# Performance work log

Measured on AMD Instinct MI355X. Metric: run time of the kernel, lower is better.

## Reference

```python
import jax, jax.numpy as jnp
import numpy as np

N_G = 50000   # glomeruli nodes
N_C = 100000  # immune cell nodes
D_IN = 128    # raw input feature dim
D = 64        # hidden_dim
E_GG = 800000
E_CG = 1600000
E_CC = 1600000
LN_EPS = 1e-5


def _ln(x, s, b):
    m = x.mean(-1, keepdims=True)
    v = ((x - m) ** 2).mean(-1, keepdims=True)
    return (x - m) * jax.lax.rsqrt(v + LN_EPS) * s + b


def _gcn(x, ei, ew, W, b, n):
    # PyG GCNConv: normalize=True, add_self_loops=True (self-loop weight 1)
    xt = x @ W                                   # [n, D]
    row, col = ei[0], ei[1]
    deg = jax.ops.segment_sum(ew, col, num_segments=n) + 1.0  # + self loop
    dinv = jnp.where(deg > 0, jax.lax.rsqrt(deg), 0.0)
    norm = dinv[row] * ew * dinv[col]            # [E]
    out = jax.ops.segment_sum(norm[:, None] * xt[row], col, num_segments=n)
    out = out + (dinv * dinv)[:, None] * xt      # self-loop contribution
    return out + b


def _gin(x_src, x_dst, ei, eps, W, b, n_dst):
    # PyG GINConv (bipartite): nn((1+eps)*x_dst + sum_j x_src[j]), nn = Linear+ReLU
    agg = jax.ops.segment_sum(x_src[ei[0]], ei[1], num_segments=n_dst)
    h = (1.0 + eps) * x_dst + agg
    return jax.nn.relu(h @ W + b)


def setup_inputs() -> dict:
    key = jax.random.key(0)
    ks = jax.random.split(key, 48)
    ctr = [0]
    def nk():
        k = ks[ctr[0]]; ctr[0] += 1; return k
    def w(fan_in, shape):
        return jax.random.normal(nk(), shape, jnp.float32) * (1.0 / np.sqrt(fan_in))
    inp = {}
    inp["x_glom"] = jax.random.normal(nk(), (N_G, D_IN), jnp.float32)
    inp["x_cell"] = jax.random.normal(nk(), (N_C, D_IN), jnp.float32)
    inp["edge_index_gg"] = jax.random.randint(nk(), (2, E_GG), 0, N_G)
    inp["edge_weight_gg"] = jax.random.uniform(nk(), (E_GG,), jnp.float32)
    inp["edge_index_cg"] = jnp.stack([jax.random.randint(nk(), (E_CG,), 0, N_C),
                                      jax.random.randint(nk(), (E_CG,), 0, N_G)])
    inp["edge_index_cc"] = jax.random.randint(nk(), (2, E_CC), 0, N_C)
    # initial per-node-type FC (LazyLinear -> LayerNorm -> ReLU)
    inp["W_in_g"] = w(D_IN, (D_IN, D)); inp["b_in_g"] = jnp.zeros((D,))
    inp["lnig_s"] = jnp.ones((D,));     inp["lnig_b"] = jnp.zeros((D,))
    inp["W_in_c"] = w(D_IN, (D_IN, D)); inp["b_in_c"] = jnp.zeros((D,))
    inp["lnic_s"] = jnp.ones((D,));     inp["lnic_b"] = jnp.zeros((D,))
    for l in ("1", "2"):
        inp["W_gcn" + l] = w(D, (D, D)); inp["b_gcn" + l] = jnp.zeros((D,))
        inp["eps_cg" + l] = jnp.zeros((1,))
        inp["W_cg" + l] = w(D, (D, D)); inp["b_cg" + l] = jnp.zeros((D,))
        inp["eps_cc" + l] = jnp.zeros((1,))
        inp["W_cc" + l] = w(D, (D, D)); inp["b_cc" + l] = jnp.zeros((D,))
        inp["ln" + l + "_s"] = jnp.ones((D,)); inp["ln" + l + "_b"] = jnp.zeros((D,))
    inp["W_out"] = w(D, (D, 3)); inp["b_out"] = jnp.zeros((3,))
    return inp


def reference(x_glom, x_cell, edge_index_gg, edge_weight_gg, edge_index_cg, edge_index_cc,
              W_in_g, b_in_g, lnig_s, lnig_b, W_in_c, b_in_c, lnic_s, lnic_b,
              W_gcn1, b_gcn1, eps_cg1, W_cg1, b_cg1, eps_cc1, W_cc1, b_cc1, ln1_s, ln1_b,
              W_gcn2, b_gcn2, eps_cg2, W_cg2, b_cg2, eps_cc2, W_cc2, b_cc2, ln2_s, ln2_b,
              W_out, b_out):
    # initial per-type FC (dropout identity in eval)
    xg = jax.nn.relu(_ln(x_glom @ W_in_g + b_in_g, lnig_s, lnig_b))
    xc = jax.nn.relu(_ln(x_cell @ W_in_c + b_in_c, lnic_s, lnic_b))
    # hetero MP layer 1: HeteroConv aggr='sum' over relations into each dst type
    g = _gcn(xg, edge_index_gg, edge_weight_gg, W_gcn1, b_gcn1, N_G) \
        + _gin(xc, xg, edge_index_cg, eps_cg1, W_cg1, b_cg1, N_G)
    c = _gin(xc, xc, edge_index_cc, eps_cc1, W_cc1, b_cc1, N_C)
    xg = jax.nn.relu(_ln(g, ln1_s, ln1_b))   # shared LayerNorm across node types
    xc = jax.nn.relu(_ln(c, ln1_s, ln1_b))
    # hetero MP layer 2
    g = _gcn(xg, edge_index_gg, edge_weight_gg, W_gcn2, b_gcn2, N_G) \
        + _gin(xc, xg, edge_index_cg, eps_cg2, W_cg2, b_cg2, N_G)
    c = _gin(xc, xc, edge_index_cc, eps_cc2, W_cc2, b_cc2, N_C)
    xg = jax.nn.relu(_ln(g, ln2_s, ln2_b))
    xc = jax.nn.relu(_ln(c, ln2_s, ln2_b))
    logits = xg @ W_out + b_out
    return jax.nn.softmax(logits, axis=-1)
```

## Files before the change

### kernel.cpp

```cpp
#include <hip/hip_runtime.h>
#include <hip/hip_fp16.h>

#define NG 50000
#define NC 100000
#define DIN 128
#define D 64
#define EGG 800000
#define ECG 1600000
#define ECC 1600000
#define LN_EPS 1e-5f

#define SCAN_N (2 * NG + NC)
#define E_ALL (EGG + ECG + ECC)
#define NBKT 196
#define NBLK 512
#define EPB ((E_ALL + NBLK - 1) / NBLK)

typedef _Float16 f16x8 __attribute__((ext_vector_type(8)));
typedef float f32x4 __attribute__((ext_vector_type(4)));

__device__ __forceinline__ float wave_sum64(float v) {
#pragma unroll
  for (int off = 32; off > 0; off >>= 1) v += __shfl_xor(v, off);
  return v;
}

__device__ __forceinline__ float bcast_lane(float v, int k) {
  return __int_as_float(__builtin_amdgcn_readlane(__float_as_int(v), k));
}

__device__ __forceinline__ float csr_gather_s2(
    const int* __restrict__ src, const float* __restrict__ nrm,
    const __half* __restrict__ tab, int e0, int e1, int lane) {
  int h = lane >> 5;
  int m = lane & 31;
  float ax0 = 0.f, ax1 = 0.f, ax2 = 0.f, ax3 = 0.f;
  float ay0 = 0.f, ay1 = 0.f, ay2 = 0.f, ay3 = 0.f;
  for (int e = e0; e < e1; e += 16) {
#pragma unroll
    for (int p = 0; p < 8; ++p) {
      int i0 = e + 2 * p;
      int se = src[i0];
      int so = src[i0 + 1];
      int s = h ? so : se;
      bool valid = (i0 + h) < e1;
      float w;
      if (nrm) {
        float we = nrm[i0], wo = nrm[i0 + 1];
        w = h ? wo : we;
      } else {
        w = 1.0f;
      }
      w = valid ? w : 0.0f;
      s = valid ? s : 0;
      __half2 v = *(const __half2*)(tab + (size_t)s * D + 2 * m);
      float vl = __low2float(v), vh = __high2float(v);
      switch (p & 3) {
        case 0: ax0 = fmaf(w, vl, ax0); ay0 = fmaf(w, vh, ay0); break;
        case 1: ax1 = fmaf(w, vl, ax1); ay1 = fmaf(w, vh, ay1); break;
        case 2: ax2 = fmaf(w, vl, ax2); ay2 = fmaf(w, vh, ay2); break;
        default: ax3 = fmaf(w, vl, ax3); ay3 = fmaf(w, vh, ay3); break;
      }
    }
  }
  float ax = (ax0 + ax1) + (ax2 + ax3);
  float ay = (ay0 + ay1) + (ay2 + ay3);
  ax += __shfl_xor(ax, 32);
  ay += __shfl_xor(ay, 32);
  float ev = __shfl(ax, lane >> 1);
  float od = __shfl(ay, lane >> 1);
  return (lane & 1) ? od : ev;
}

__global__ __launch_bounds__(256) void fc_in_mfma_kernel(
    const float* __restrict__ x, const float* __restrict__ W,
    const float* __restrict__ b, const float* __restrict__ s,
    const float* __restrict__ beta, __half* __restrict__ y, int n) {
  int wid = (int)(((size_t)blockIdx.x * blockDim.x + threadIdx.x) >> 6);
  int lane = threadIdx.x & 63;
  int r0 = wid * 16;
  if (r0 >= n) return;
  int lo = lane & 15;
  int hi = lane >> 4;

  f16x8 bf[4][4];
#pragma unroll
  for (int kk = 0; kk < 4; ++kk) {
    int kbase = kk * 32 + hi * 8;
#pragma unroll
    for (int t = 0; t < 4; ++t) {
      int c = t * 16 + lo;
      f16x8 v;
#pragma unroll
      for (int j = 0; j < 8; ++j)
        v[j] = (_Float16)W[(kbase + j) * 64 + c];
      bf[kk][t] = v;
    }
  }

  f32x4 acc[4];
#pragma unroll
  for (int t = 0; t < 4; ++t) acc[t] = (f32x4){0.f, 0.f, 0.f, 0.f};

  const float* xr = x + (size_t)(r0 + lo) * DIN;
#pragma unroll
  for (int kk = 0; kk < 4; ++kk) {
    int kbase = kk * 32 + hi * 8;
    float4 xa = *(const float4*)(xr + kbase);
    float4 xb = *(const float4*)(xr + kbase + 4);
    f16x8 af;
    af[0] = (_Float16)xa.x; af[1] = (_Float16)xa.y;
    af[2] = (_Float16)xa.z; af[3] = (_Float16)xa.w;
    af[4] = (_Float16)xb.x; af[5] = (_Float16)xb.y;
    af[6] = (_Float16)xb.z; af[7] = (_Float16)xb.w;
#pragma unroll
    for (int t = 0; t < 4; ++t)
      acc[t] = __builtin_amdgcn_mfma_f32_16x16x32_f16(af, bf[kk][t], acc[t], 0, 0, 0);
  }

  float bc[4], lsv[4], lbv[4];
#pragma unroll
  for (int t = 0; t < 4; ++t) {
    int c = t * 16 + lo;
    bc[t] = b[c]; lsv[t] = s[c]; lbv[t] = beta[c];
  }
#pragma unroll
  for (int reg = 0; reg < 4; ++reg) {
    float v[4];
    float s1 = 0.0f;
#pragma unroll
    for (int t = 0; t < 4; ++t) { v[t] = acc[t][reg] + bc[t]; s1 += v[t]; }
#pragma unroll
    for (int off = 1; off < 16; off <<= 1) s1 += __shfl_xor(s1, off);
    float m = s1 * (1.0f / 64.0f);
    float s2 = 0.0f;
#pragma unroll
    for (int t = 0; t < 4; ++t) { float d = v[t] - m; s2 += d * d; }
#pragma unroll
    for (int off = 1; off < 16; off <<= 1) s2 += __shfl_xor(s2, off);
    float rinv = rsqrtf(s2 * (1.0f / 64.0f) + LN_EPS);
    int r = r0 + hi * 4 + reg;
#pragma unroll
    for (int t = 0; t < 4; ++t) {
      float o = (v[t] - m) * rinv * lsv[t] + lbv[t];
      y[(size_t)r * D + t * 16 + lo] = __float2half(fmaxf(o, 0.0f));
    }
  }
}

__global__ __launch_bounds__(256) void r1_hist_kernel(
    const int* __restrict__ ei_gg, const int* __restrict__ ei_cg,
    const int* __restrict__ ei_cc, int* __restrict__ bhist,
    int* __restrict__ btot) {
  __shared__ int hist[256];
  int t = threadIdx.x;
  int k = blockIdx.x;
  hist[t] = 0;
  __syncthreads();
  int base = k * EPB;
  for (int i = t; i < EPB; i += 256) {
    int e = base + i;
    if (e >= E_ALL) break;
    int key;
    if (e < EGG) key = ei_gg[EGG + e];
    else if (e < EGG + ECG) key = NG + ei_cg[ECG + (e - EGG)];
    else key = 2 * NG + ei_cc[ECC + (e - EGG - ECG)];
    atomicAdd(&hist[key >> 10], 1);
  }
  __syncthreads();
  if (t < NBKT) {
    bhist[t * NBLK + k] = hist[t];
    atomicAdd(&btot[t], hist[t]);
  }
}

__global__ __launch_bounds__(256) void r2b_kernel(
    const int* __restrict__ btot, int* __restrict__ bbase,
    int* __restrict__ S) {
  __shared__ int sh[256];
  int t = threadIdx.x;
  int v = (t < NBKT) ? btot[t] : 0;
  sh[t] = v;
  __syncthreads();
#pragma unroll
  for (int off = 1; off < 256; off <<= 1) {
    int u = (t >= off) ? sh[t - off] : 0;
    __syncthreads();
    sh[t] += u;
    __syncthreads();
  }
  if (t < NBKT) bbase[t] = sh[t] - v;
  if (t == 255) { bbase[NBKT] = sh[255]; S[SCAN_N] = sh[255]; }
}

__global__ __launch_bounds__(512) void r2c_kernel(
    const int* __restrict__ bhist, const int* __restrict__ bbase,
    int* __restrict__ base) {
  int b = blockIdx.x;
  int t = threadIdx.x;
  int lane = t & 63, wv = t >> 6;
  int v = bhist[b * NBLK + t];
  int sc = v;
#pragma unroll
  for (int off = 1; off < 64; off <<= 1) {
    int u = __shfl_up(sc, off);
    if (lane >= off) sc += u;
  }
  __shared__ int ws[8];
  if (lane == 63) ws[wv] = sc;
  __syncthreads();
  int wb = 0;
  for (int i = 0; i < wv; ++i) wb += ws[i];
  base[b * NBLK + t] = bbase[b] + wb + sc - v;
}

__global__ __launch_bounds__(256) void r3_scatter_kernel(
    const int* __restrict__ ei_gg, const float* __restrict__ ew_gg,
    const int* __restrict__ ei_cg, const int* __restrict__ ei_cc,
    const int* __restrict__ base, int* __restrict__ ssort,
    float* __restrict__ wsort) {
  __shared__ int cur[256];
  int t = threadIdx.x;
  int k = blockIdx.x;
  if (t < NBKT) cur[t] = base[t * NBLK + k];
  __syncthreads();
  int bb = k * EPB;
  for (int i = t; i < EPB; i += 256) {
    int e = bb + i;
    if (e >= E_ALL) break;
    int key, s; float w = 0.0f; bool isg = false;
    if (e < EGG) {
      key = ei_gg[EGG + e]; s = ei_gg[e]; w = ew_gg[e]; isg = true;
    } else if (e < EGG + ECG) {
      int q = e - EGG; key = NG + ei_cg[ECG + q]; s = ei_cg[q];
    } else {
      int q = e - EGG - ECG; key = 2 * NG + ei_cc[ECC + q]; s = ei_cc[q];
    }
    int p = atomicAdd(&cur[key >> 10], 1);
    ssort[p] = ((key & 1023) << 17) | s;
    if (isg) wsort[p] = w;
  }
}

__global__ __launch_bounds__(1024) void r4_sort_kernel(
    const int* __restrict__ ssort, const float* __restrict__ wsort,
    const int* __restrict__ bbase, int* __restrict__ S,
    int* __restrict__ srcbuf, float* __restrict__ ewp) {
  int b = blockIdx.x;
  int t = threadIdx.x;
  int e0 = bbase[b], e1 = bbase[b + 1];
  int kbase = b << 10;
  __shared__ int hist[1024];
  __shared__ int sh[1024];
  __shared__ int cur[1024];
  hist[t] = 0;
  __syncthreads();
  for (int e = e0 + t; e < e1; e += 1024)
    atomicAdd(&hist[((unsigned)ssort[e]) >> 17], 1);
  __syncthreads();
  int c = hist[t];
  sh[t] = c;
  __syncthreads();
#pragma unroll
  for (int off = 1; off < 1024; off <<= 1) {
    int u = (t >= off) ? sh[t - off] : 0;
    __syncthreads();
    sh[t] += u;
    __syncthreads();
  }
  int ex = e0 + sh[t] - c;
  int key = kbase + t;
  if (key < SCAN_N) S[key] = ex;
  cur[t] = ex;
  __syncthreads();
  for (int e = e0 + t; e < e1; e += 1024) {
    int rec = ssort[e];
    int lk = ((unsigned)rec) >> 17;
    int p = atomicAdd(&cur[lk], 1);
    srcbuf[p] = rec & 0x1FFFF;
    if (kbase + lk < NG) ewp[p] = wsort[e];
  }
}

__global__ __launch_bounds__(256) void deg_kernel(
    const int* __restrict__ S, const float* __restrict__ ewp,
    float* __restrict__ dinv) {
  int i = (int)(((size_t)blockIdx.x * blockDim.x + threadIdx.x) >> 6);
  int lane = threadIdx.x & 63;
  if (i >= NG) return;
  int e0 = S[i], e1 = S[i + 1];
  float s = 0.0f;
  for (int e = e0 + lane; e < e1; e += 64) s += ewp[e];
  s = wave_sum64(s);
  if (lane == 0) dinv[i] = rsqrtf(s + 1.0f);
}

__global__ __launch_bounds__(256) void nrm_kernel(
    const int* __restrict__ S, const int* __restrict__ srcbuf,
    const float* __restrict__ ewp, const float* __restrict__ dinv,
    float* __restrict__ nrm) {
  int i = (int)(((size_t)blockIdx.x * blockDim.x + threadIdx.x) >> 6);
  int lane = threadIdx.x & 63;
  if (i >= NG) return;
  float di = dinv[i];
  int e0 = S[i], e1 = S[i + 1];
  for (int e = e0 + lane; e < e1; e += 64)
    nrm[e] = dinv[srcbuf[e]] * ewp[e] * di;
}

__global__ __launch_bounds__(256) void glom_layer_kernel(
    const int* __restrict__ rp_gg, const int* __restrict__ rp_cg,
    const int* __restrict__ srcbuf, const float* __restrict__ nrm_gg,
    const __half* __restrict__ xg_old, const __half* __restrict__ xc_old,
    const float* __restrict__ dinv,
    const float* __restrict__ W_gcn, const float* __restrict__ b_gcn,
    const float* __restrict__ eps_cg, const float* __restrict__ W_cg,
    const float* __restrict__ b_cg,
    const float* __restrict__ ls, const float* __restrict__ lb,
    __half* __restrict__ xg_new, int n) {
  int i = (int)(((size_t)blockIdx.x * blockDim.x + threadIdx.x) >> 6);
  int lane = threadIdx.x & 63;
  if (i >= n) return;
  int iu = __builtin_amdgcn_readfirstlane(i);
  int ge0 = __builtin_amdgcn_readfirstlane(rp_gg[iu]);
  int ge1 = __builtin_amdgcn_readfirstlane(rp_gg[iu + 1]);
  int fe0 = __builtin_amdgcn_readfirstlane(rp_cg[iu]);
  int fe1 = __builtin_amdgcn_readfirstlane(rp_cg[iu + 1]);
  float self = __half2float(xg_old[(size_t)iu * D + lane]);
  float di = dinv[iu];
  float accG = di * di * self
             + csr_gather_s2(srcbuf, nrm_gg, xg_old, ge0, ge1, lane);
  float accC = csr_gather_s2(srcbuf, nullptr, xc_old, fe0, fe1, lane);
  float gcn = b_gcn[lane];
#pragma unroll
  for (int k = 0; k < 64; ++k)
    gcn = fmaf(bcast_lane(accG, k), W_gcn[k * 64 + lane], gcn);
  float h = (1.0f + eps_cg[0]) * self + accC;
  float gin = b_cg[lane];
#pragma unroll
  for (int k = 0; k < 64; ++k)
    gin = fmaf(bcast_lane(h, k), W_cg[k * 64 + lane], gin);
  float g = gcn + fmaxf(gin, 0.0f);
  float m = wave_sum64(g) * (1.0f / 64.0f);
  float d = g - m;
  float var = wave_sum64(d * d) * (1.0f / 64.0f);
  float o = d * rsqrtf(var + LN_EPS) * ls[lane] + lb[lane];
  xg_new[(size_t)iu * D + lane] = __float2half(fmaxf(o, 0.0f));
}

__global__ __launch_bounds__(256) void cell_layer_kernel(
    const int* __restrict__ rp_cc, const int* __restrict__ srcbuf,
    const __half* __restrict__ xc_old,
    const float* __restrict__ eps_cc, const float* __restrict__ W_cc,
    const float* __restrict__ b_cc,
    const float* __restrict__ ls, const float* __restrict__ lb,
    __half* __restrict__ xc_new, int n) {
  int i = (int)(((size_t)blockIdx.x * blockDim.x + threadIdx.x) >> 6);
  int lane = threadIdx.x & 63;
  if (i >= n) return;
  int iu = __builtin_amdgcn_readfirstlane(i);
  int e0 = __builtin_amdgcn_readfirstlane(rp_cc[iu]);
  int e1 = __builtin_amdgcn_readfirstlane(rp_cc[iu + 1]);
  float self = __half2float(xc_old[(size_t)iu * D + lane]);
  float acc = csr_gather_s2(srcbuf, nullptr, xc_old, e0, e1, lane);
  float h = (1.0f + eps_cc[0]) * self + acc;
  float gin = b_cc[lane];
#pragma unroll
  for (int k = 0; k < 64; ++k)
    gin = fmaf(bcast_lane(h, k), W_cc[k * 64 + lane], gin);
  float g = fmaxf(gin, 0.0f);
  float m = wave_sum64(g) * (1.0f / 64.0f);
  float d = g - m;
  float var = wave_sum64(d * d) * (1.0f / 64.0f);
  float o = d * rsqrtf(var + LN_EPS) * ls[lane] + lb[lane];
  xc_new[(size_t)iu * D + lane] = __float2half(fmaxf(o, 0.0f));
}

__global__ __launch_bounds__(256) void out_kernel(
    const __half* __restrict__ xg, const float* __restrict__ W,
    const float* __restrict__ b, float* __restrict__ out, int n) {
  int wid = (int)(((size_t)blockIdx.x * blockDim.x + threadIdx.x) >> 6);
  int lane = threadIdx.x & 63;
  if (wid >= n) return;
  float v = __half2float(xg[(size_t)wid * D + lane]);
  float a0 = wave_sum64(v * W[lane * 3 + 0]) + b[0];
  float a1 = wave_sum64(v * W[lane * 3 + 1]) + b[1];
  float a2 = wave_sum64(v * W[lane * 3 + 2]) + b[2];
  float m = fmaxf(a0, fmaxf(a1, a2));
  float e0 = expf(a0 - m), e1 = expf(a1 - m), e2 = expf(a2 - m);
  float inv = 1.0f / (e0 + e1 + e2);
  if (lane == 0) {
    out[(size_t)wid * 3 + 0] = e0 * inv;
    out[(size_t)wid * 3 + 1] = e1 * inv;
    out[(size_t)wid * 3 + 2] = e2 * inv;
  }
}

extern "C" void kernel_launch(void* const* d_in, const int* in_sizes, int n_in,
                              void* d_out, int out_size, void* d_ws, size_t ws_size,
                              hipStream_t stream) {
  const float* x_glom = (const float*)d_in[0];
  const float* x_cell = (const float*)d_in[1];
  const int*   ei_gg  = (const int*)d_in[2];
  const float* ew_gg  = (const float*)d_in[3];
  const int*   ei_cg  = (const int*)d_in[4];
  const int*   ei_cc  = (const int*)d_in[5];
  const float* W_in_g = (const float*)d_in[6];
  const float* b_in_g = (const float*)d_in[7];
  const float* lnig_s = (const float*)d_in[8];
  const float* lnig_b = (const float*)d_in[9];
  const float* W_in_c = (const float*)d_in[10];
  const float* b_in_c = (const float*)d_in[11];
  const float* lnic_s = (const float*)d_in[12];
  const float* lnic_b = (const float*)d_in[13];
  const float* W_outp = (const float*)d_in[34];
  const float* b_outp = (const float*)d_in[35];

  char* P = (char*)d_ws;
  __half* xg0 = (__half*)P;                    P += (size_t)NG * D * 2;
  __half* xg1 = (__half*)P;                    P += (size_t)NG * D * 2;
  __half* xc0 = (__half*)P;                    P += (size_t)NC * D * 2;
  __half* xc1 = (__half*)P;                    P += (size_t)NC * D * 2;
  float* dinv = (float*)P;                     P += (size_t)NG * 4;
  float* nrm  = (float*)P;                     P += (size_t)EGG * 4;
  int* S      = (int*)P;                       P += (size_t)(SCAN_N + 1) * 4;
  int* srcbuf = (int*)P;                       P += (size_t)E_ALL * 4;
  int* bhist  = (int*)P;                       P += (size_t)NBKT * NBLK * 4;
  int* base   = (int*)P;                       P += (size_t)NBKT * NBLK * 4;
  int* btot   = (int*)P;                       P += (size_t)NBKT * 4;
  int* bbase  = (int*)P;                       P += (size_t)(NBKT + 1) * 4;
  int* ssort   = (int*)d_ws;
  float* wsort = (float*)(ssort + E_ALL);
  float* ewp   = wsort + EGG;

  dim3 blk(256);
  auto wgrid = [](long long waves) { return dim3((unsigned)((waves + 3) / 4)); };

  hipMemsetAsync(btot, 0, NBKT * sizeof(int), stream);
  r1_hist_kernel<<<dim3(NBLK), blk, 0, stream>>>(ei_gg, ei_cg, ei_cc, bhist, btot);
  r2b_kernel<<<dim3(1), dim3(256), 0, stream>>>(btot, bbase, S);
  r2c_kernel<<<dim3(NBKT), dim3(512), 0, stream>>>(bhist, bbase, base);
  r3_scatter_kernel<<<dim3(NBLK), blk, 0, stream>>>(
      ei_gg, ew_gg, ei_cg, ei_cc, base, ssort, wsort);
  r4_sort_kernel<<<dim3(NBKT), dim3(1024), 0, stream>>>(
      ssort, wsort, bbase, S, srcbuf, ewp);
  deg_kernel<<<wgrid(NG), blk, 0, stream>>>(S, ewp, dinv);
  nrm_kernel<<<wgrid(NG), blk, 0, stream>>>(S, srcbuf, ewp, dinv, nrm);

  fc_in_mfma_kernel<<<wgrid(NG / 16), blk, 0, stream>>>(
      x_glom, W_in_g, b_in_g, lnig_s, lnig_b, xg0, NG);
  fc_in_mfma_kernel<<<wgrid(NC / 16), blk, 0, stream>>>(
      x_cell, W_in_c, b_in_c, lnic_s, lnic_b, xc0, NC);

  const int* rp_gg = S;
  const int* rp_cg = S + NG;
  const int* rp_cc = S + 2 * NG;
  __half* xg_cur = xg0; __half* xg_nxt = xg1;
  __half* xc_cur = xc0; __half* xc_nxt = xc1;
  for (int l = 0; l < 2; ++l) {
    const float* const* p = (const float* const*)(d_in + 14 + 10 * l);
    const float* W_gcn = p[0]; const float* b_gcn = p[1];
    const float* eps_cg = p[2]; const float* W_cg = p[3]; const float* b_cg = p[4];
    const float* eps_cc = p[5]; const float* W_cc = p[6]; const float* b_cc = p[7];
    const float* ln_s = p[8]; const float* ln_b = p[9];

    glom_layer_kernel<<<wgrid(NG), blk, 0, stream>>>(
        rp_gg, rp_cg, srcbuf, nrm, xg_cur, xc_cur, dinv,
        W_gcn, b_gcn, eps_cg, W_cg, b_cg, ln_s, ln_b, xg_nxt, NG);
    cell_layer_kernel<<<wgrid(NC), blk, 0, stream>>>(
        rp_cc, srcbuf, xc_cur, eps_cc, W_cc, b_cc, ln_s, ln_b, xc_nxt, NC);

    __half* t;
    t = xg_cur; xg_cur = xg_nxt; xg_nxt = t;
    t = xc_cur; xc_cur = xc_nxt; xc_nxt = t;
  }

  out_kernel<<<wgrid(NG), blk, 0, stream>>>(xg_cur, W_outp, b_outp, (float*)d_out, NG);
}
```

Baseline: 474.2 us.

## Use MFMA for per-node dense transforms via shared-memory staging in layer kernels

The glom and cell layer kernels now run 16 waves per 1024-thread block. Each wave gathers one node's aggregate and stages it as fp16 in shared memory, then a single wave computes the 16x64 by 64x64 products with 16x16x32 f16 MFMA instructions and a LayerNorm reduced across lanes. This replaces the 64-step readlane/FMA loop per node. The cost is fp16 rounding of the aggregates, a block barrier, and 15 of 16 waves sitting idle during the epilogue while each block holds a large slot.

```diff
diff --git a/kernel.cpp b/kernel.cpp
--- a/kernel.cpp
+++ b/kernel.cpp
@@ -23,10 +23,6 @@
 #pragma unroll
   for (int off = 32; off > 0; off >>= 1) v += __shfl_xor(v, off);
   return v;
-}
-
-__device__ __forceinline__ float bcast_lane(float v, int k) {
-  return __int_as_float(__builtin_amdgcn_readlane(__float_as_int(v), k));
 }
 
 __device__ __forceinline__ float csr_gather_s2(
@@ -72,6 +68,13 @@
   return (lane & 1) ? od : ev;
 }
 
+__device__ __forceinline__ f16x8 ldB(const float* __restrict__ W, int kbase, int c) {
+  f16x8 v;
+#pragma unroll
+  for (int j = 0; j < 8; ++j) v[j] = (_Float16)W[(kbase + j) * 64 + c];
+  return v;
+}
+
 __global__ __launch_bounds__(256) void fc_in_mfma_kernel(
     const float* __restrict__ x, const float* __restrict__ W,
     const float* __restrict__ b, const float* __restrict__ s,
@@ -88,14 +91,7 @@
   for (int kk = 0; kk < 4; ++kk) {
     int kbase = kk * 32 + hi * 8;
 #pragma unroll
-    for (int t = 0; t < 4; ++t) {
-      int c = t * 16 + lo;
-      f16x8 v;
-#pragma unroll
-      for (int j = 0; j < 8; ++j)
-        v[j] = (_Float16)W[(kbase + j) * 64 + c];
-      bf[kk][t] = v;
-    }
+    for (int t = 0; t < 4; ++t) bf[kk][t] = ldB(W, kbase, t * 16 + lo);
   }
 
   f32x4 acc[4];
@@ -308,7 +304,7 @@
     nrm[e] = dinv[srcbuf[e]] * ewp[e] * di;
 }
 
-__global__ __launch_bounds__(256) void glom_layer_kernel(
+__global__ __launch_bounds__(1024) void glom_layer_kernel(
     const int* __restrict__ rp_gg, const int* __restrict__ rp_cg,
     const int* __restrict__ srcbuf, const float* __restrict__ nrm_gg,
     const __half* __restrict__ xg_old, const __half* __restrict__ xc_old,
@@ -317,11 +313,13 @@
     const float* __restrict__ eps_cg, const float* __restrict__ W_cg,
     const float* __restrict__ b_cg,
     const float* __restrict__ ls, const float* __restrict__ lb,
-    __half* __restrict__ xg_new, int n) {
-  int i = (int)(((size_t)blockIdx.x * blockDim.x + threadIdx.x) >> 6);
+    __half* __restrict__ xg_new) {
+  __shared__ __align__(16) _Float16 A1[16][72];
+  __shared__ __align__(16) _Float16 A2[16][72];
+  int wv = threadIdx.x >> 6;
   int lane = threadIdx.x & 63;
-  if (i >= n) return;
-  int iu = __builtin_amdgcn_readfirstlane(i);
+  int iu = __builtin_amdgcn_readfirstlane(blockIdx.x * 16 + wv);
+
   int ge0 = __builtin_amdgcn_readfirstlane(rp_gg[iu]);
   int ge1 = __builtin_amdgcn_readfirstlane(rp_gg[iu + 1]);
   int fe0 = __builtin_amdgcn_readfirstlane(rp_cg[iu]);
@@ -331,49 +329,136 @@
   float accG = di * di * self
              + csr_gather_s2(srcbuf, nrm_gg, xg_old, ge0, ge1, lane);
   float accC = csr_gather_s2(srcbuf, nullptr, xc_old, fe0, fe1, lane);
-  float gcn = b_gcn[lane];
-#pragma unroll
-  for (int k = 0; k < 64; ++k)
-    gcn = fmaf(bcast_lane(accG, k), W_gcn[k * 64 + lane], gcn);
   float h = (1.0f + eps_cg[0]) * self + accC;
-  float gin = b_cg[lane];
-#pragma unroll
-  for (int k = 0; k < 64; ++k)
-    gin = fmaf(bcast_lane(h, k), W_cg[k * 64 + lane], gin);
-  float g = gcn + fmaxf(gin, 0.0f);
-  float m = wave_sum64(g) * (1.0f / 64.0f);
-  float d = g - m;
-  float var = wave_sum64(d * d) * (1.0f / 64.0f);
-  float o = d * rsqrtf(var + LN_EPS) * ls[lane] + lb[lane];
-  xg_new[(size_t)iu * D + lane] = __float2half(fmaxf(o, 0.0f));
-}
-
-__global__ __launch_bounds__(256) void cell_layer_kernel(
+  A1[wv][lane] = (_Float16)accG;
+  A2[wv][lane] = (_Float16)h;
+  __syncthreads();
+  if (wv != 0) return;
+
+  int lo = lane & 15;
+  int hi = lane >> 4;
+  f16x8 a1[2], a2[2];
+#pragma unroll
+  for (int kk = 0; kk < 2; ++kk) {
+    a1[kk] = *(const f16x8*)&A1[lo][kk * 32 + hi * 8];
+    a2[kk] = *(const f16x8*)&A2[lo][kk * 32 + hi * 8];
+  }
+  f32x4 c1[4], c2[4];
+#pragma unroll
+  for (int t = 0; t < 4; ++t) {
+    int c = t * 16 + lo;
+    f32x4 acc = (f32x4){0.f, 0.f, 0.f, 0.f};
+#pragma unroll
+    for (int kk = 0; kk < 2; ++kk)
+      acc = __builtin_amdgcn_mfma_f32_16x16x32_f16(a1[kk], ldB(W_gcn, kk * 32 + hi * 8, c), acc, 0, 0, 0);
+    c1[t] = acc;
+    acc = (f32x4){0.f, 0.f, 0.f, 0.f};
+#pragma unroll
+    for (int kk = 0; kk < 2; ++kk)
+      acc = __builtin_amdgcn_mfma_f32_16x16x32_f16(a2[kk], ldB(W_cg, kk * 32 + hi * 8, c), acc, 0, 0, 0);
+    c2[t] = acc;
+  }
+  float bc1[4], bc2[4], lsv[4], lbv[4];
+#pragma unroll
+  for (int t = 0; t < 4; ++t) {
+    int c = t * 16 + lo;
+    bc1[t] = b_gcn[c]; bc2[t] = b_cg[c]; lsv[t] = ls[c]; lbv[t] = lb[c];
+  }
+#pragma unroll
+  for (int reg = 0; reg < 4; ++reg) {
+    float v[4];
+    float s1 = 0.0f;
+#pragma unroll
+    for (int t = 0; t < 4; ++t) {
+      v[t] = (c1[t][reg] + bc1[t]) + fmaxf(c2[t][reg] + bc2[t], 0.0f);
+      s1 += v[t];
+    }
+#pragma unroll
+    for (int off = 1; off < 16; off <<= 1) s1 += __shfl_xor(s1, off);
+    float m = s1 * (1.0f / 64.0f);
+    float s2 = 0.0f;
+#pragma unroll
+    for (int t = 0; t < 4; ++t) { float d = v[t] - m; s2 += d * d; }
+#pragma unroll
+    for (int off = 1; off < 16; off <<= 1) s2 += __shfl_xor(s2, off);
+    float rinv = rsqrtf(s2 * (1.0f / 64.0f) + LN_EPS);
+    int r = blockIdx.x * 16 + hi * 4 + reg;
+#pragma unroll
+    for (int t = 0; t < 4; ++t) {
+      float o = (v[t] - m) * rinv * lsv[t] + lbv[t];
+      xg_new[(size_t)r * D + t * 16 + lo] = __float2half(fmaxf(o, 0.0f));
+    }
+  }
+}
+
+__global__ __launch_bounds__(1024) void cell_layer_kernel(
     const int* __restrict__ rp_cc, const int* __restrict__ srcbuf,
     const __half* __restrict__ xc_old,
     const float* __restrict__ eps_cc, const float* __restrict__ W_cc,
     const float* __restrict__ b_cc,
     const float* __restrict__ ls, const float* __restrict__ lb,
-    __half* __restrict__ xc_new, int n) {
-  int i = (int)(((size_t)blockIdx.x * blockDim.x + threadIdx.x) >> 6);
+    __half* __restrict__ xc_new) {
+  __shared__ __align__(16) _Float16 A2[16][72];
+  int wv = threadIdx.x >> 6;
   int lane = threadIdx.x & 63;
-  if (i >= n) return;
-  int iu = __builtin_amdgcn_readfirstlane(i);
+  int iu = __builtin_amdgcn_readfirstlane(blockIdx.x * 16 + wv);
+
   int e0 = __builtin_amdgcn_readfirstlane(rp_cc[iu]);
   int e1 = __builtin_amdgcn_readfirstlane(rp_cc[iu + 1]);
   float self = __half2float(xc_old[(size_t)iu * D + lane]);
   float acc = csr_gather_s2(srcbuf, nullptr, xc_old, e0, e1, lane);
   float h = (1.0f + eps_cc[0]) * self + acc;
-  float gin = b_cc[lane];
-#pragma unroll
-  for (int k = 0; k < 64; ++k)
-    gin = fmaf(bcast_lane(h, k), W_cc[k * 64 + lane], gin);
-  float g = fmaxf(gin, 0.0f);
-  float m = wave_sum64(g) * (1.0f / 64.0f);
-  float d = g - m;
-  float var = wave_sum64(d * d) * (1.0f / 64.0f);
-  float o = d * rsqrtf(var + LN_EPS) * ls[lane] + lb[lane];
-  xc_new[(size_t)iu * D + lane] = __float2half(fmaxf(o, 0.0f));
+  A2[wv][lane] = (_Float16)h;
+  __syncthreads();
+  if (wv != 0) return;
+
+  int lo = lane & 15;
+  int hi = lane >> 4;
+  f16x8 a2[2];
+#pragma unroll
+  for (int kk = 0; kk < 2; ++kk)
+    a2[kk] = *(const f16x8*)&A2[lo][kk * 32 + hi * 8];
+  f32x4 c2[4];
+#pragma unroll
+  for (int t = 0; t < 4; ++t) {
+    int c = t * 16 + lo;
+    f32x4 a = (f32x4){0.f, 0.f, 0.f, 0.f};
+#pragma unroll
+    for (int kk = 0; kk < 2; ++kk)
+      a = __builtin_amdgcn_mfma_f32_16x16x32_f16(a2[kk], ldB(W_cc, kk * 32 + hi * 8, c), a, 0, 0, 0);
+    c2[t] = a;
+  }
+  float bc2[4], lsv[4], lbv[4];
+#pragma unroll
+  for (int t = 0; t < 4; ++t) {
+    int c = t * 16 + lo;
+    bc2[t] = b_cc[c]; lsv[t] = ls[c]; lbv[t] = lb[c];
+  }
+#pragma unroll
+  for (int reg = 0; reg < 4; ++reg) {
+    float v[4];
+    float s1 = 0.0f;
+#pragma unroll
+    for (int t = 0; t < 4; ++t) {
+      v[t] = fmaxf(c2[t][reg] + bc2[t], 0.0f);
+      s1 += v[t];
+    }
+#pragma unroll
+    for (int off = 1; off < 16; off <<= 1) s1 += __shfl_xor(s1, off);
+    float m = s1 * (1.0f / 64.0f);
+    float s2 = 0.0f;
+#pragma unroll
+    for (int t = 0; t < 4; ++t) { float d = v[t] - m; s2 += d * d; }
+#pragma unroll
+    for (int off = 1; off < 16; off <<= 1) s2 += __shfl_xor(s2, off);
+    float rinv = rsqrtf(s2 * (1.0f / 64.0f) + LN_EPS);
+    int r = blockIdx.x * 16 + hi * 4 + reg;
+#pragma unroll
+    for (int t = 0; t < 4; ++t) {
+      float o = (v[t] - m) * rinv * lsv[t] + lbv[t];
+      xc_new[(size_t)r * D + t * 16 + lo] = __float2half(fmaxf(o, 0.0f));
+    }
+  }
 }
 
 __global__ __launch_bounds__(256) void out_kernel(
@@ -464,11 +549,11 @@
     const float* eps_cc = p[5]; const float* W_cc = p[6]; const float* b_cc = p[7];
     const float* ln_s = p[8]; const float* ln_b = p[9];
 
-    glom_layer_kernel<<<wgrid(NG), blk, 0, stream>>>(
+    glom_layer_kernel<<<dim3(NG / 16), dim3(1024), 0, stream>>>(
         rp_gg, rp_cg, srcbuf, nrm, xg_cur, xc_cur, dinv,
-        W_gcn, b_gcn, eps_cg, W_cg, b_cg, ln_s, ln_b, xg_nxt, NG);
-    cell_layer_kernel<<<wgrid(NC), blk, 0, stream>>>(
-        rp_cc, srcbuf, xc_cur, eps_cc, W_cc, b_cc, ln_s, ln_b, xc_nxt, NC);
+        W_gcn, b_gcn, eps_cg, W_cg, b_cg, ln_s, ln_b, xg_nxt);
+    cell_layer_kernel<<<dim3(NC / 16), dim3(1024), 0, stream>>>(
+        rp_cc, srcbuf, xc_cur, eps_cc, W_cc, b_cc, ln_s, ln_b, xc_nxt);
 
     __half* t;
     t = xg_cur; xg_cur = xg_nxt; xg_nxt = t;
```

After: 474.9 us. About the same (+0.1%).
